# Kernel optimization log

Measured on AMD Instinct MI355X. Metric: run time of the kernel, lower is better.

The kernel has to match this reference:

```python
import jax, jax.numpy as jnp
import numpy as np

B, S, D, H = 4, 2048, 1024, 16
DH = D // H


def setup_inputs() -> dict:
    key = jax.random.key(0)
    ks = jax.random.split(key, 12)
    s = 0.02
    inp = {
        "q": jax.random.normal(ks[0], (B, S, D), jnp.float32),
        "k": jax.random.normal(ks[1], (B, S, D), jnp.float32),
        "v": jax.random.normal(ks[2], (B, S, D), jnp.float32),
        # causal mask, broadcastable over batch and heads (mask==0 -> -1e9)
        "mask": jnp.tril(jnp.ones((S, S), jnp.int32))[None, None, :, :],
        "wq": jax.random.normal(ks[3], (D, D), jnp.float32) * s,
        "bq": jnp.zeros((D,), jnp.float32),
        "wk": jax.random.normal(ks[4], (D, D), jnp.float32) * s,
        "bk": jnp.zeros((D,), jnp.float32),
        "wv": jax.random.normal(ks[5], (D, D), jnp.float32) * s,
        "bv": jnp.zeros((D,), jnp.float32),
        "wo": jax.random.normal(ks[6], (D, D), jnp.float32) * s,
        "bo": jnp.zeros((D,), jnp.float32),
    }
    return inp


def reference(q, k, v, mask, wq, bq, wk, bk, wv, bv, wo, bo):
    # linear projections (torch Linear: x @ W^T + b)
    qh = (q @ wq.T + bq).reshape(B, S, H, DH).transpose(0, 2, 1, 3)  # [B,H,S,DH]
    kh = (k @ wk.T + bk).reshape(B, S, H, DH).transpose(0, 2, 1, 3)
    vh = (v @ wv.T + bv).reshape(B, S, H, DH).transpose(0, 2, 1, 3)
    scale = 1.0 / jnp.sqrt(jnp.float32(DH))
    score = jnp.einsum("bhqd,bhkd->bhqk", qh, kh) * scale  # [B,H,S,S]
    score = jnp.where(mask == 0, jnp.float32(-1e9), score)
    attn = jax.nn.softmax(score, axis=-1)
    ctx = jnp.einsum("bhqk,bhkd->bhqd", attn, vh)  # [B,H,S,DH]
    ctx = ctx.transpose(0, 2, 1, 3).reshape(B, S, D)
    return ctx @ wo.T + bo
```

## Files before the change

### kernel.cpp

```cpp
#include <hip/hip_runtime.h>
#include <hip/hip_bf16.h>

#define NB 4
#define NS 2048
#define ND 1024
#define NH 16
#define NDH 64
#define E_ 8388608
#define W_ 1048576

typedef __attribute__((ext_vector_type(8))) __bf16 bf16x8;
typedef __attribute__((ext_vector_type(4))) float f32x4;
typedef __attribute__((ext_vector_type(2))) unsigned int u32x2;
typedef unsigned short us16;
typedef unsigned int u32;

__device__ __forceinline__ unsigned short f2bf(float f) {
  union { float f; unsigned u; } v; v.f = f;
  unsigned r = v.u + 0x7FFFu + ((v.u >> 16) & 1u);
  return (unsigned short)(r >> 16);
}

typedef const __attribute__((address_space(1))) unsigned int* gas_t;
typedef __attribute__((address_space(3))) unsigned int* las_t;
__device__ __forceinline__ void gl2lds16(const void* g, void* l) {
  __builtin_amdgcn_global_load_lds((gas_t)g, (las_t)l, 16, 0, 0);
}

__global__ __launch_bounds__(256) void conv_bf16(
    const float* __restrict__ q, const float* __restrict__ k, const float* __restrict__ v,
    const float* __restrict__ wq, const float* __restrict__ wk, const float* __restrict__ wv,
    const float* __restrict__ wo,
    us16* __restrict__ qb, us16* __restrict__ kb, us16* __restrict__ vb,
    us16* __restrict__ wqb, us16* __restrict__ wkb, us16* __restrict__ wvb,
    us16* __restrict__ wob)
{
  int b = blockIdx.x;
  int seg, off;
  if (b < 24576) { seg = b >> 13; off = b & 8191; }
  else { b -= 24576; seg = 3 + (b >> 10); off = b & 1023; }
  const float* s; us16* d;
  switch (seg) {
    case 0: s = q;  d = qb;  break;
    case 1: s = k;  d = kb;  break;
    case 2: s = v;  d = vb;  break;
    case 3: s = wq; d = wqb; break;
    case 4: s = wk; d = wkb; break;
    case 5: s = wv; d = wvb; break;
    default: s = wo; d = wob; break;
  }
  size_t idx = ((size_t)off * 256 + threadIdx.x) * 4;
  float4 f = *(const float4*)(s + idx);
  ushort4 u;
  u.x = f2bf(f.x); u.y = f2bf(f.y); u.z = f2bf(f.z); u.w = f2bf(f.w);
  *(ushort4*)(d + idx) = u;
}

__global__ __launch_bounds__(256, 3) void gemm_proj3(
    const us16* __restrict__ A0, const us16* __restrict__ A1, const us16* __restrict__ A2,
    const us16* __restrict__ W0, const us16* __restrict__ W1, const us16* __restrict__ W2,
    const float* __restrict__ b0, const float* __restrict__ b1, const float* __restrict__ b2,
    us16* __restrict__ o0, us16* __restrict__ o1, us16* __restrict__ o2,
    float qscale, int s0, int s1, int s2)
{
  const int seg = (blockIdx.z == 0) ? s0 : (blockIdx.z == 1) ? s1 : s2;
  const us16* A  = (blockIdx.z == 0) ? A0 : (blockIdx.z == 1) ? A1 : A2;
  const us16* Wt = (blockIdx.z == 0) ? W0 : (blockIdx.z == 1) ? W1 : W2;
  const float* bias = (blockIdx.z == 0) ? b0 : (blockIdx.z == 1) ? b1 : b2;
  us16* out = (blockIdx.z == 0) ? o0 : (blockIdx.z == 1) ? o1 : o2;
  const float scale = (seg == 0) ? qscale : 1.0f;

  __shared__ us16 As[128][64];
  __shared__ us16 Bs[128][64];
  const int tid = threadIdx.x;
  const int lane = tid & 63;
  const int w = tid >> 6;
  const int l15 = lane & 15, quad = lane >> 4;
  const int sw = l15 & 7;
  const int rowBase = blockIdx.x * 128, colBase = blockIdx.y * 128;
  const int srow = w * 32 + (lane >> 3);
  const int cu = (lane & 7) ^ ((lane >> 3) & 7);
  const us16* ga = A  + (size_t)(rowBase + srow) * ND + cu * 8;
  const us16* gb = Wt + (size_t)(colBase + srow) * ND + cu * 8;
  const int wr = (w >> 1) * 64, wc = (w & 1) * 64;

  f32x4 acc[4][4] = {};
  for (int kt = 0; kt < ND; kt += 64) {
    __syncthreads();
    #pragma unroll
    for (int c = 0; c < 4; ++c) {
      gl2lds16(ga + kt + c * 8 * ND, &As[w * 32 + c * 8][0]);
      gl2lds16(gb + kt + c * 8 * ND, &Bs[w * 32 + c * 8][0]);
    }
    __syncthreads();
    #pragma unroll
    for (int ks = 0; ks < 2; ++ks) {
      bf16x8 af[4], bfr[4];
      #pragma unroll
      for (int i = 0; i < 4; ++i)
        af[i]  = *(const bf16x8*)&As[wr + i * 16 + l15][((ks * 4 + quad) ^ sw) * 8];
      #pragma unroll
      for (int j = 0; j < 4; ++j)
        bfr[j] = *(const bf16x8*)&Bs[wc + j * 16 + l15][((ks * 4 + quad) ^ sw) * 8];
      #pragma unroll
      for (int i = 0; i < 4; ++i)
        #pragma unroll
        for (int j = 0; j < 4; ++j)
          acc[i][j] = __builtin_amdgcn_mfma_f32_16x16x32_bf16(af[i], bfr[j], acc[i][j], 0, 0, 0);
    }
  }

  if (seg < 2) {
    #pragma unroll
    for (int i = 0; i < 4; ++i) {
      #pragma unroll
      for (int j = 0; j < 4; ++j) {
        int colg = colBase + wc + j * 16 + l15;
        float bval = bias[colg];
        #pragma unroll
        for (int r = 0; r < 4; ++r) {
          int rowg = rowBase + wr + i * 16 + quad * 4 + r;
          out[(size_t)rowg * ND + colg] = f2bf((acc[i][j][r] + bval) * scale);
        }
      }
    }
  } else {
    #pragma unroll
    for (int i = 0; i < 4; ++i) {
      #pragma unroll
      for (int j = 0; j < 4; ++j) {
        int colg = colBase + wc + j * 16 + l15;
        float bval = bias[colg];
        int h_ = colg >> 6, d_ = colg & 63;
        int rowg0 = rowBase + wr + i * 16 + quad * 4;
        int b_ = rowg0 >> 11, sr0 = rowg0 & (NS - 1);
        ushort4 vv;
        vv.x = f2bf(acc[i][j][0] + bval);
        vv.y = f2bf(acc[i][j][1] + bval);
        vv.z = f2bf(acc[i][j][2] + bval);
        vv.w = f2bf(acc[i][j][3] + bval);
        *(ushort4*)(out + ((size_t)(b_ * NH + h_) * NDH + d_) * NS + sr0) = vv;
      }
    }
  }
}

__global__ __launch_bounds__(256, 4) void attn(
    const us16* __restrict__ Qh, const us16* __restrict__ Kh,
    const us16* __restrict__ Vht, us16* __restrict__ ctx)
{
  __shared__ us16 Ks[2][64][64];
  __shared__ us16 Vts[2][64][64];
  __shared__ us16 Ps[4][32][32];
  us16* Qsta = &Vts[0][0][0];

  const int bh = blockIdx.x & 63;
  const int pr = blockIdx.x >> 6;
  const int b_ = bh >> 4, h_ = bh & 15;
  const int tid = threadIdx.x, lane = tid & 63, w = tid >> 6;
  const int l15 = lane & 15, quad = lane >> 4;
  const int sw = l15 & 7;
  const int lr8 = lane >> 3;
  const int cu = (lane & 7) ^ (lr8 & 7);

  bf16x8 ones;
  #pragma unroll
  for (int i = 0; i < 8; ++i) ones[i] = (__bf16)1.0f;

  const us16* gkbase = Kh  + ((size_t)b_ * NS + w * 16 + lr8) * ND + h_ * NDH + cu * 8;
  const us16* gvbase = Vht + ((size_t)bh * NDH + w * 16 + lr8) * NS + cu * 8;

  for (int pass = 0; pass < 2; ++pass) {
    const int tq = pass ? (15 - pr) : pr;
    const int qb0 = tq * 128;
    const int nt = tq * 2 + 2;
    const int qw = qb0 + w * 32;

    __syncthreads();
    {
      const us16* gq = Qh + ((size_t)b_ * NS + qb0 + w * 32 + lr8) * ND + h_ * NDH + cu * 8;
      #pragma unroll
      for (int u = 0; u < 4; ++u)
        gl2lds16(gq + (size_t)u * 8 * ND, Qsta + (w * 32 + u * 8) * 64);
    }
    __syncthreads();
    bf16x8 bq[2][2];
    #pragma unroll
    for (int ntl = 0; ntl < 2; ++ntl)
      #pragma unroll
      for (int c = 0; c < 2; ++c)
        bq[ntl][c] = *(const bf16x8*)(Qsta + (w * 32 + ntl * 16 + l15) * 64 +
                                      (((c * 4 + quad) ^ sw) * 8));
    __syncthreads();

    gl2lds16(gkbase,            &Ks[0][w * 16][0]);
    gl2lds16(gkbase + 8 * ND,   &Ks[0][w * 16 + 8][0]);
    gl2lds16(gvbase,            &Vts[0][w * 16][0]);
    gl2lds16(gvbase + 8 * NS,   &Vts[0][w * 16 + 8][0]);

    f32x4 o[2][4] = {};
    f32x4 o_l[2] = {};

    for (int it = 0; it < nt; ++it) {
      const int kb = it * 64;
      const int cur = it & 1;
      __syncthreads();
      if (it + 1 < nt) {
        const int nxt = cur ^ 1;
        gl2lds16(gkbase + (size_t)(kb + 64) * ND,          &Ks[nxt][w * 16][0]);
        gl2lds16(gkbase + (size_t)(kb + 72) * ND,          &Ks[nxt][w * 16 + 8][0]);
        gl2lds16(gvbase + kb + 64,                         &Vts[nxt][w * 16][0]);
        gl2lds16(gvbase + kb + 64 + 8 * NS,                &Vts[nxt][w * 16 + 8][0]);
      }
      if (kb <= qw + 31) {
        const bool full = (kb + 63 <= qw);
        #pragma unroll
        for (int h2 = 0; h2 < 2; ++h2) {
          f32x4 s[2][2];
          #pragma unroll
          for (int mt = 0; mt < 2; ++mt) {
            bf16x8 ak0 = *(const bf16x8*)&Ks[cur][h2 * 32 + mt * 16 + l15][(quad ^ sw) * 8];
            bf16x8 ak1 = *(const bf16x8*)&Ks[cur][h2 * 32 + mt * 16 + l15][((4 + quad) ^ sw) * 8];
            #pragma unroll
            for (int ntl = 0; ntl < 2; ++ntl) {
              f32x4 t = {};
              t = __builtin_amdgcn_mfma_f32_16x16x32_bf16(ak0, bq[ntl][0], t, 0, 0, 0);
              t = __builtin_amdgcn_mfma_f32_16x16x32_bf16(ak1, bq[ntl][1], t, 0, 0, 0);
              s[mt][ntl] = t;
            }
          }
          #pragma unroll
          for (int mt = 0; mt < 2; ++mt)
            #pragma unroll
            for (int ntl = 0; ntl < 2; ++ntl) {
              u32 u[4];
              if (full) {
                #pragma unroll
                for (int r = 0; r < 4; ++r)
                  u[r] = __float_as_uint(__builtin_amdgcn_exp2f(s[mt][ntl][r]));
              } else {
                const int keyb = kb + h2 * 32 + mt * 16 + quad * 4;
                const int qg = qw + ntl * 16 + l15;
                #pragma unroll
                for (int r = 0; r < 4; ++r) {
                  float p = (keyb + r <= qg) ? __builtin_amdgcn_exp2f(s[mt][ntl][r]) : 0.f;
                  u[r] = __float_as_uint(p);
                }
              }
              u32 lo = (u[0] >> 16) | (u[1] & 0xffff0000u);
              u32 hi = (u[2] >> 16) | (u[3] & 0xffff0000u);
              int uswz = (mt * 2 + (quad >> 1)) ^ (l15 & 3);
              *(u32x2*)&Ps[w][ntl * 16 + l15][uswz * 8 + (quad & 1) * 4] = (u32x2){lo, hi};
            }
          bf16x8 bv[4];
          #pragma unroll
          for (int n = 0; n < 4; ++n)
            bv[n] = *(const bf16x8*)&Vts[cur][n * 16 + l15][((h2 * 4 + quad) ^ sw) * 8];
          #pragma unroll
          for (int ntl = 0; ntl < 2; ++ntl) {
            bf16x8 ap = *(const bf16x8*)&Ps[w][ntl * 16 + l15][(quad ^ (l15 & 3)) * 8];
            o_l[ntl] = __builtin_amdgcn_mfma_f32_16x16x32_bf16(ap, ones, o_l[ntl], 0, 0, 0);
            #pragma unroll
            for (int n = 0; n < 4; ++n)
              o[ntl][n] = __builtin_amdgcn_mfma_f32_16x16x32_bf16(ap, bv[n], o[ntl][n], 0, 0, 0);
          }
        }
      }
    }

    #pragma unroll
    for (int ntl = 0; ntl < 2; ++ntl) {
      #pragma unroll
      for (int r = 0; r < 4; ++r) {
        float inv = __builtin_amdgcn_rcpf(o_l[ntl][r]);
        int qg = qb0 + w * 32 + ntl * 16 + quad * 4 + r;
        us16* dst = ctx + ((size_t)b_ * NS + qg) * ND + h_ * NDH;
        #pragma unroll
        for (int n = 0; n < 4; ++n)
          dst[n * 16 + l15] = f2bf(o[ntl][n][r] * inv);
      }
    }
  }
}

__global__ __launch_bounds__(256, 3) void gemm_out(
    const us16* __restrict__ A, const us16* __restrict__ Wt,
    const float* __restrict__ bias, float* __restrict__ out)
{
  __shared__ us16 As[128][64];
  __shared__ us16 Bs[128][64];
  const int tid = threadIdx.x;
  const int lane = tid & 63;
  const int w = tid >> 6;
  const int l15 = lane & 15, quad = lane >> 4;
  const int sw = l15 & 7;
  const int rowBase = blockIdx.x * 128, colBase = blockIdx.y * 128;
  const int srow = w * 32 + (lane >> 3);
  const int cu = (lane & 7) ^ ((lane >> 3) & 7);
  const us16* ga = A  + (size_t)(rowBase + srow) * ND + cu * 8;
  const us16* gb = Wt + (size_t)(colBase + srow) * ND + cu * 8;
  const int wr = (w >> 1) * 64, wc = (w & 1) * 64;

  f32x4 acc[4][4] = {};
  for (int kt = 0; kt < ND; kt += 64) {
    __syncthreads();
    #pragma unroll
    for (int c = 0; c < 4; ++c) {
      gl2lds16(ga + kt + c * 8 * ND, &As[w * 32 + c * 8][0]);
      gl2lds16(gb + kt + c * 8 * ND, &Bs[w * 32 + c * 8][0]);
    }
    __syncthreads();
    #pragma unroll
    for (int ks = 0; ks < 2; ++ks) {
      bf16x8 af[4], bfr[4];
      #pragma unroll
      for (int i = 0; i < 4; ++i)
        af[i]  = *(const bf16x8*)&As[wr + i * 16 + l15][((ks * 4 + quad) ^ sw) * 8];
      #pragma unroll
      for (int j = 0; j < 4; ++j)
        bfr[j] = *(const bf16x8*)&Bs[wc + j * 16 + l15][((ks * 4 + quad) ^ sw) * 8];
      #pragma unroll
      for (int i = 0; i < 4; ++i)
        #pragma unroll
        for (int j = 0; j < 4; ++j)
          acc[i][j] = __builtin_amdgcn_mfma_f32_16x16x32_bf16(af[i], bfr[j], acc[i][j], 0, 0, 0);
    }
  }

  #pragma unroll
  for (int i = 0; i < 4; ++i) {
    #pragma unroll
    for (int j = 0; j < 4; ++j) {
      int colg = colBase + wc + j * 16 + l15;
      float bval = bias[colg];
      #pragma unroll
      for (int r = 0; r < 4; ++r) {
        int rowg = rowBase + wr + i * 16 + quad * 4 + r;
        out[(size_t)rowg * ND + colg] = acc[i][j][r] + bval;
      }
    }
  }
}

extern "C" void kernel_launch(void* const* d_in, const int* in_sizes, int n_in,
                              void* d_out, int out_size, void* d_ws, size_t ws_size,
                              hipStream_t stream) {
  const float* q  = (const float*)d_in[0];
  const float* k  = (const float*)d_in[1];
  const float* v  = (const float*)d_in[2];
  const float* wq = (const float*)d_in[4];
  const float* bq_ = (const float*)d_in[5];
  const float* wk = (const float*)d_in[6];
  const float* bk_ = (const float*)d_in[7];
  const float* wv = (const float*)d_in[8];
  const float* bv_ = (const float*)d_in[9];
  const float* wo = (const float*)d_in[10];
  const float* bo_ = (const float*)d_in[11];

  us16* ws = (us16*)d_ws;
  us16* qb  = ws;
  us16* kb  = ws + (size_t)E_;
  us16* vb  = ws + (size_t)2 * E_;
  us16* wqb = ws + (size_t)3 * E_;
  us16* wkb = wqb + W_;
  us16* wvb = wkb + W_;
  us16* wob = wvb + W_;
  us16* KhF = wob + W_;
  us16* ctx = vb;
  us16* Vht = (us16*)d_out;
  us16* Qh  = (us16*)d_out + (size_t)E_;

  const float qscale = 0.125f * 1.44269504088896340736f;
  const bool fused = ws_size >= ((size_t)4 * E_ + 4 * W_) * 2;

  conv_bf16<<<28672, 256, 0, stream>>>(q, k, v, wq, wk, wv, wo,
                                       qb, kb, vb, wqb, wkb, wvb, wob);
  if (fused) {
    gemm_proj3<<<dim3(64, 8, 3), 256, 0, stream>>>(
        qb, kb, vb, wqb, wkb, wvb, bq_, bk_, bv_, Qh, KhF, Vht, qscale, 0, 1, 2);
    attn<<<512, 256, 0, stream>>>(Qh, KhF, Vht, ctx);
  } else {
    gemm_proj3<<<dim3(64, 8, 2), 256, 0, stream>>>(
        qb, vb, vb, wqb, wvb, wvb, bq_, bv_, bv_, Qh, Vht, Vht, qscale, 0, 2, 2);
    gemm_proj3<<<dim3(64, 8, 1), 256, 0, stream>>>(
        kb, kb, kb, wkb, wkb, wkb, bk_, bk_, bk_, qb, qb, qb, qscale, 1, 1, 1);
    attn<<<512, 256, 0, stream>>>(Qh, qb, Vht, ctx);
  }
  gemm_out<<<dim3(64, 8), 256, 0, stream>>>(ctx, wob, bo_, (float*)d_out);
}
```

Measured before the change: 317.5 us.

## Widen attention key tiles to 128 and overlap first K/V load with Q staging

The attention kernel now processes 128 keys per iteration instead of 64. This halves the number of barrier-separated iterations and doubles the double-buffered K/V LDS footprint, so launch bounds drop to 2 blocks per SM. The first K/V tile load is issued together with the Q staging load, removing one barrier, and Q now stages into the second V buffer. It also adds s_setprio around the MFMA sections and changes the V LDS swizzle to fit the wider row layout. The trade-off is lower occupancy and more causal-skip granularity work per wave.

```diff
diff --git a/kernel.cpp b/kernel.cpp
--- a/kernel.cpp
+++ b/kernel.cpp
@@ -145,14 +145,14 @@
   }
 }
 
-__global__ __launch_bounds__(256, 4) void attn(
+__global__ __launch_bounds__(256, 2) void attn(
     const us16* __restrict__ Qh, const us16* __restrict__ Kh,
     const us16* __restrict__ Vht, us16* __restrict__ ctx)
 {
-  __shared__ us16 Ks[2][64][64];
-  __shared__ us16 Vts[2][64][64];
+  __shared__ us16 Ks[2][128][64];
+  __shared__ us16 Vts[2][64][128];
   __shared__ us16 Ps[4][32][32];
-  us16* Qsta = &Vts[0][0][0];
+  us16* Qsta = &Vts[1][0][0];
 
   const int bh = blockIdx.x & 63;
   const int pr = blockIdx.x >> 6;
@@ -162,18 +162,23 @@
   const int sw = l15 & 7;
   const int lr8 = lane >> 3;
   const int cu = (lane & 7) ^ (lr8 & 7);
+  const int vr = lane >> 4;
+  const int vs = lane & 15;
+  const int cs0 = (vs & 8) | ((vs & 7) ^ vr);
+  const int cs1 = (vs & 8) | ((vs & 7) ^ (vr | 4));
 
   bf16x8 ones;
   #pragma unroll
   for (int i = 0; i < 8; ++i) ones[i] = (__bf16)1.0f;
 
-  const us16* gkbase = Kh  + ((size_t)b_ * NS + w * 16 + lr8) * ND + h_ * NDH + cu * 8;
-  const us16* gvbase = Vht + ((size_t)bh * NDH + w * 16 + lr8) * NS + cu * 8;
+  const us16* gk  = Kh  + ((size_t)b_ * NS + w * 32 + lr8) * ND + h_ * NDH + cu * 8;
+  const us16* gv0 = Vht + ((size_t)bh * NDH + w * 16 + vr) * NS + cs0 * 8;
+  const us16* gv1 = Vht + ((size_t)bh * NDH + w * 16 + 4 + vr) * NS + cs1 * 8;
 
   for (int pass = 0; pass < 2; ++pass) {
     const int tq = pass ? (15 - pr) : pr;
     const int qb0 = tq * 128;
-    const int nt = tq * 2 + 2;
+    const int nt = tq + 1;
     const int qw = qb0 + w * 32;
 
     __syncthreads();
@@ -183,6 +188,13 @@
       for (int u = 0; u < 4; ++u)
         gl2lds16(gq + (size_t)u * 8 * ND, Qsta + (w * 32 + u * 8) * 64);
     }
+    #pragma unroll
+    for (int u = 0; u < 4; ++u)
+      gl2lds16(gk + (size_t)(u * 8) * ND, &Ks[0][w * 32 + u * 8][0]);
+    gl2lds16(gv0,          &Vts[0][w * 16][0]);
+    gl2lds16(gv1,          &Vts[0][w * 16 + 4][0]);
+    gl2lds16(gv0 + 8 * NS, &Vts[0][w * 16 + 8][0]);
+    gl2lds16(gv1 + 8 * NS, &Vts[0][w * 16 + 12][0]);
     __syncthreads();
     bf16x8 bq[2][2];
     #pragma unroll
@@ -191,80 +203,82 @@
       for (int c = 0; c < 2; ++c)
         bq[ntl][c] = *(const bf16x8*)(Qsta + (w * 32 + ntl * 16 + l15) * 64 +
                                       (((c * 4 + quad) ^ sw) * 8));
-    __syncthreads();
-
-    gl2lds16(gkbase,            &Ks[0][w * 16][0]);
-    gl2lds16(gkbase + 8 * ND,   &Ks[0][w * 16 + 8][0]);
-    gl2lds16(gvbase,            &Vts[0][w * 16][0]);
-    gl2lds16(gvbase + 8 * NS,   &Vts[0][w * 16 + 8][0]);
 
     f32x4 o[2][4] = {};
     f32x4 o_l[2] = {};
 
     for (int it = 0; it < nt; ++it) {
-      const int kb = it * 64;
+      const int kb = it * 128;
       const int cur = it & 1;
       __syncthreads();
       if (it + 1 < nt) {
         const int nxt = cur ^ 1;
-        gl2lds16(gkbase + (size_t)(kb + 64) * ND,          &Ks[nxt][w * 16][0]);
-        gl2lds16(gkbase + (size_t)(kb + 72) * ND,          &Ks[nxt][w * 16 + 8][0]);
-        gl2lds16(gvbase + kb + 64,                         &Vts[nxt][w * 16][0]);
-        gl2lds16(gvbase + kb + 64 + 8 * NS,                &Vts[nxt][w * 16 + 8][0]);
-      }
-      if (kb <= qw + 31) {
-        const bool full = (kb + 63 <= qw);
-        #pragma unroll
-        for (int h2 = 0; h2 < 2; ++h2) {
-          f32x4 s[2][2];
+        const int kn = kb + 128;
+        #pragma unroll
+        for (int u = 0; u < 4; ++u)
+          gl2lds16(gk + (size_t)(kn + u * 8) * ND, &Ks[nxt][w * 32 + u * 8][0]);
+        gl2lds16(gv0 + kn,          &Vts[nxt][w * 16][0]);
+        gl2lds16(gv1 + kn,          &Vts[nxt][w * 16 + 4][0]);
+        gl2lds16(gv0 + kn + 8 * NS, &Vts[nxt][w * 16 + 8][0]);
+        gl2lds16(gv1 + kn + 8 * NS, &Vts[nxt][w * 16 + 12][0]);
+      }
+      #pragma unroll
+      for (int h2 = 0; h2 < 4; ++h2) {
+        const int keyb0 = kb + h2 * 32;
+        if (keyb0 > qw + 31) continue;
+        const bool full = (keyb0 + 31 <= qw);
+        f32x4 s[2][2];
+        __builtin_amdgcn_s_setprio(1);
+        #pragma unroll
+        for (int mt = 0; mt < 2; ++mt) {
+          bf16x8 ak0 = *(const bf16x8*)&Ks[cur][h2 * 32 + mt * 16 + l15][(quad ^ sw) * 8];
+          bf16x8 ak1 = *(const bf16x8*)&Ks[cur][h2 * 32 + mt * 16 + l15][((4 + quad) ^ sw) * 8];
           #pragma unroll
-          for (int mt = 0; mt < 2; ++mt) {
-            bf16x8 ak0 = *(const bf16x8*)&Ks[cur][h2 * 32 + mt * 16 + l15][(quad ^ sw) * 8];
-            bf16x8 ak1 = *(const bf16x8*)&Ks[cur][h2 * 32 + mt * 16 + l15][((4 + quad) ^ sw) * 8];
-            #pragma unroll
-            for (int ntl = 0; ntl < 2; ++ntl) {
-              f32x4 t = {};
-              t = __builtin_amdgcn_mfma_f32_16x16x32_bf16(ak0, bq[ntl][0], t, 0, 0, 0);
-              t = __builtin_amdgcn_mfma_f32_16x16x32_bf16(ak1, bq[ntl][1], t, 0, 0, 0);
-              s[mt][ntl] = t;
+          for (int ntl = 0; ntl < 2; ++ntl) {
+            f32x4 t = {};
+            t = __builtin_amdgcn_mfma_f32_16x16x32_bf16(ak0, bq[ntl][0], t, 0, 0, 0);
+            t = __builtin_amdgcn_mfma_f32_16x16x32_bf16(ak1, bq[ntl][1], t, 0, 0, 0);
+            s[mt][ntl] = t;
+          }
+        }
+        __builtin_amdgcn_s_setprio(0);
+        #pragma unroll
+        for (int mt = 0; mt < 2; ++mt)
+          #pragma unroll
+          for (int ntl = 0; ntl < 2; ++ntl) {
+            u32 u[4];
+            if (full) {
+              #pragma unroll
+              for (int r = 0; r < 4; ++r)
+                u[r] = __float_as_uint(__builtin_amdgcn_exp2f(s[mt][ntl][r]));
+            } else {
+              const int keyb = keyb0 + mt * 16 + quad * 4;
+              const int qg = qw + ntl * 16 + l15;
+              #pragma unroll
+              for (int r = 0; r < 4; ++r) {
+                float p = (keyb + r <= qg) ? __builtin_amdgcn_exp2f(s[mt][ntl][r]) : 0.f;
+                u[r] = __float_as_uint(p);
+              }
             }
+            u32 lo = (u[0] >> 16) | (u[1] & 0xffff0000u);
+            u32 hi = (u[2] >> 16) | (u[3] & 0xffff0000u);
+            int uswz = (mt * 2 + (quad >> 1)) ^ (l15 & 3);
+            *(u32x2*)&Ps[w][ntl * 16 + l15][uswz * 8 + (quad & 1) * 4] = (u32x2){lo, hi};
           }
-          #pragma unroll
-          for (int mt = 0; mt < 2; ++mt)
-            #pragma unroll
-            for (int ntl = 0; ntl < 2; ++ntl) {
-              u32 u[4];
-              if (full) {
-                #pragma unroll
-                for (int r = 0; r < 4; ++r)
-                  u[r] = __float_as_uint(__builtin_amdgcn_exp2f(s[mt][ntl][r]));
-              } else {
-                const int keyb = kb + h2 * 32 + mt * 16 + quad * 4;
-                const int qg = qw + ntl * 16 + l15;
-                #pragma unroll
-                for (int r = 0; r < 4; ++r) {
-                  float p = (keyb + r <= qg) ? __builtin_amdgcn_exp2f(s[mt][ntl][r]) : 0.f;
-                  u[r] = __float_as_uint(p);
-                }
-              }
-              u32 lo = (u[0] >> 16) | (u[1] & 0xffff0000u);
-              u32 hi = (u[2] >> 16) | (u[3] & 0xffff0000u);
-              int uswz = (mt * 2 + (quad >> 1)) ^ (l15 & 3);
-              *(u32x2*)&Ps[w][ntl * 16 + l15][uswz * 8 + (quad & 1) * 4] = (u32x2){lo, hi};
-            }
-          bf16x8 bv[4];
+        bf16x8 bv[4];
+        #pragma unroll
+        for (int n = 0; n < 4; ++n)
+          bv[n] = *(const bf16x8*)&Vts[cur][n * 16 + l15][((h2 * 4 + quad) ^ sw) * 8];
+        __builtin_amdgcn_s_setprio(1);
+        #pragma unroll
+        for (int ntl = 0; ntl < 2; ++ntl) {
+          bf16x8 ap = *(const bf16x8*)&Ps[w][ntl * 16 + l15][(quad ^ (l15 & 3)) * 8];
+          o_l[ntl] = __builtin_amdgcn_mfma_f32_16x16x32_bf16(ap, ones, o_l[ntl], 0, 0, 0);
           #pragma unroll
           for (int n = 0; n < 4; ++n)
-            bv[n] = *(const bf16x8*)&Vts[cur][n * 16 + l15][((h2 * 4 + quad) ^ sw) * 8];
-          #pragma unroll
-          for (int ntl = 0; ntl < 2; ++ntl) {
-            bf16x8 ap = *(const bf16x8*)&Ps[w][ntl * 16 + l15][(quad ^ (l15 & 3)) * 8];
-            o_l[ntl] = __builtin_amdgcn_mfma_f32_16x16x32_bf16(ap, ones, o_l[ntl], 0, 0, 0);
-            #pragma unroll
-            for (int n = 0; n < 4; ++n)
-              o[ntl][n] = __builtin_amdgcn_mfma_f32_16x16x32_bf16(ap, bv[n], o[ntl][n], 0, 0, 0);
-          }
+            o[ntl][n] = __builtin_amdgcn_mfma_f32_16x16x32_bf16(ap, bv[n], o[ntl][n], 0, 0, 0);
         }
+        __builtin_amdgcn_s_setprio(0);
       }
     }
 
```

Measured after the change: 305.4 us. 1.04x faster.
